# Performance work log

Measured on AMD Instinct MI355X. Metric: run time of the kernel, lower is better.

## Reference

```python
import jax, jax.numpy as jnp
import numpy as np

B, S, D = 4, 2048, 1024
H, DK, DV = 16, 64, 64


def setup_inputs() -> dict:
    key = jax.random.key(0)
    ks = jax.random.split(key, 7)
    scale = 0.02
    emb = jax.random.normal(ks[0], (B, S, D), dtype=jnp.float32)
    # per-head projection weights stacked over heads: [H, D, DK/DV]
    Wq = jax.random.normal(ks[1], (H, D, DK), dtype=jnp.float32) * scale
    Wk = jax.random.normal(ks[2], (H, D, DK), dtype=jnp.float32) * scale
    Wv = jax.random.normal(ks[3], (H, D, DV), dtype=jnp.float32) * scale
    # output projection (nn.Linear(d_model, d_model)): weight [D, D] (input-major) + bias
    Wo = jax.random.normal(ks[4], (D, D), dtype=jnp.float32) * scale
    bo = jax.random.normal(ks[5], (D,), dtype=jnp.float32) * scale
    return {"emb": emb, "Wq": Wq, "Wk": Wk, "Wv": Wv, "Wo": Wo, "bo": bo}


def reference(emb, Wq, Wk, Wv, Wo, bo):
    # Per-head projections, batched over heads: [B,H,S,dk]
    q = jnp.einsum("bsd,hdk->bhsk", emb, Wq)
    k = jnp.einsum("bsd,hdk->bhsk", emb, Wk)
    v = jnp.einsum("bsd,hdv->bhsv", emb, Wv)
    # Scaled dot-product with causal mask (bool_mask=True)
    scores = jnp.einsum("bhqk,bhsk->bhqs", q, k) * (DK ** -0.5)  # [B,H,S,S]
    causal = jnp.tril(jnp.ones((S, S), dtype=bool))
    scores = jnp.where(causal, scores, jnp.finfo(scores.dtype).min)
    attn = jax.nn.softmax(scores, axis=-1)
    out = jnp.einsum("bhqs,bhsv->bhqv", attn, v)  # [B,H,S,DV]
    # concat heads -> [B,S,H*DV] == [B,S,D]
    out = out.transpose(0, 2, 1, 3).reshape(B, S, H * DV)
    # output projection; dropout=0.0 -> identity
    return out @ Wo + bo
```

## Files before the change

kernel.cpp:

```cpp
#include <hip/hip_runtime.h>
#include <hip/hip_bf16.h>


typedef __attribute__((ext_vector_type(8))) short bf16x8;
typedef __attribute__((ext_vector_type(4))) float f32x4;
typedef __attribute__((ext_vector_type(4))) unsigned int u32x4;
typedef __attribute__((ext_vector_type(2))) unsigned int u32x2;

#define MFMA16(a, b, c) __builtin_amdgcn_mfma_f32_16x16x32_bf16((a), (b), (c), 0, 0, 0)

#define LOG2E 1.44269504088896340736f
#define BIG_NEG (-3.0e38f)
#define DEFER_THR 10.0f

__device__ __forceinline__ unsigned short f2bf(float f) {
  union { float f; unsigned int i; } x; x.f = f;
  unsigned int lsb = (x.i >> 16) & 1;
  x.i += 0x7fffu + lsb;
  return (unsigned short)(x.i >> 16);
}

__device__ __forceinline__ unsigned int cvtpk(float lo, float hi) {
  unsigned int r;
  asm("v_cvt_pk_bf16_f32 %0, %1, %2" : "=v"(r) : "v"(lo), "v"(hi));
  return r;
}

__device__ __forceinline__ void gl16(const unsigned short* g, void* l) {
  __builtin_amdgcn_global_load_lds(
      (const __attribute__((address_space(1))) unsigned int*)g,
      (__attribute__((address_space(3))) unsigned int*)l, 16, 0, 0);
}

__global__ void wtrans_kernel(const float* __restrict__ in,
                              unsigned short* __restrict__ out, int R, int C) {
  __shared__ unsigned short tile[32][33];
  const int bz = blockIdx.z;
  const int c0 = blockIdx.x * 32, r0 = blockIdx.y * 32;
  const float* ip = in + (size_t)bz * R * C;
  unsigned short* op = out + (size_t)bz * R * C;
  const int tx = threadIdx.x, ty = threadIdx.y;
#pragma unroll
  for (int i = 0; i < 32; i += 8)
    tile[ty + i][tx] = f2bf(ip[(size_t)(r0 + ty + i) * C + (c0 + tx)]);
  __syncthreads();
#pragma unroll
  for (int i = 0; i < 32; i += 8)
    op[(size_t)(c0 + ty + i) * R + (r0 + tx)] = tile[tx][ty + i];
}

__global__ __launch_bounds__(256)
void embconv_kernel(const float* __restrict__ in, unsigned short* __restrict__ out) {
  const int i = blockIdx.x * 256 + threadIdx.x;
  const float4 a = ((const float4*)in)[2 * i];
  const float4 b = ((const float4*)in)[2 * i + 1];
  union { unsigned short u[8]; u32x4 v; } p;
  p.u[0] = f2bf(a.x); p.u[1] = f2bf(a.y); p.u[2] = f2bf(a.z); p.u[3] = f2bf(a.w);
  p.u[4] = f2bf(b.x); p.u[5] = f2bf(b.y); p.u[6] = f2bf(b.z); p.u[7] = f2bf(b.w);
  ((u32x4*)out)[i] = p.v;
}

__global__ __launch_bounds__(256)
void qkv_kernel(const unsigned short* __restrict__ embB,
                const unsigned short* __restrict__ WqT,
                const unsigned short* __restrict__ WkT,
                const unsigned short* __restrict__ WvT,
                unsigned short* __restrict__ QG,
                unsigned short* __restrict__ KG,
                unsigned short* __restrict__ VtG) {
  const int nwg = gridDim.x;
  const int wg = blockIdx.x;
  const int swz = (wg & 7) * (nwg >> 3) + (wg >> 3);
  const int mb = swz / 24;
  const int rem = swz - mb * 24;
  const int t = rem >> 3;
  const int m0 = mb * 128;
  const int n0 = (rem & 7) * 128;
  const int b = m0 >> 11;
  const int sloc = m0 & 2047;
  const unsigned short* Wt =
      (t == 0 ? WqT : (t == 1 ? WkT : WvT)) + (size_t)(n0 >> 6) * 64 * 1024;

  __shared__ __align__(16) unsigned short As[128 * 32];
  __shared__ __align__(16) unsigned short Bs[128 * 32];

  const int tid = threadIdx.x;
  const int lane = tid & 63, w = tid >> 6;
  const int q4 = lane >> 4, l16 = lane & 15;
  const int lr = lane >> 2, lc = (lane & 3) * 8;

  f32x4 acc[4][4] = {};

  const unsigned short* ga0 = &embB[(size_t)(m0 + w * 32 + lr) * 1024 + lc];
  const unsigned short* ga1 = ga0 + 16 * 1024;
  const unsigned short* gb0 = &Wt[(size_t)(w * 32 + lr) * 1024 + lc];
  const unsigned short* gb1 = gb0 + 16 * 1024;
  char* la0 = (char*)As + w * 2048;
  char* lb0 = (char*)Bs + w * 2048;

  for (int k0 = 0; k0 < 1024; k0 += 32) {
    __syncthreads();
    gl16(ga0 + k0, la0);
    gl16(ga1 + k0, la0 + 1024);
    gl16(gb0 + k0, lb0);
    gl16(gb1 + k0, lb0 + 1024);
    __syncthreads();

    const unsigned short* PA = (t == 2) ? Bs : As;
    const unsigned short* PB = (t == 2) ? As : Bs;

    bf16x8 af[4], bfr[4];
#pragma unroll
    for (int ms = 0; ms < 4; ++ms)
      af[ms] = *(const bf16x8*)&PA[((w >> 1) * 64 + ms * 16 + l16) * 32 + q4 * 8];
#pragma unroll
    for (int js = 0; js < 4; ++js)
      bfr[js] = *(const bf16x8*)&PB[((w & 1) * 64 + js * 16 + l16) * 32 + q4 * 8];
    __builtin_amdgcn_s_setprio(1);
#pragma unroll
    for (int ms = 0; ms < 4; ++ms)
#pragma unroll
      for (int js = 0; js < 4; ++js)
        acc[ms][js] = MFMA16(af[ms], bfr[js], acc[ms][js]);
    __builtin_amdgcn_s_setprio(0);
  }

  if (t < 2) {
    unsigned short* outp = (t == 0) ? QG : KG;
    const float osc = (t == 0) ? (0.125f * LOG2E) : 1.0f;
    const int h = (n0 >> 6) + (w & 1);
    const size_t hb = (size_t)(b * 16 + h) * 2048;
#pragma unroll
    for (int ms = 0; ms < 4; ++ms)
#pragma unroll
      for (int js = 0; js < 4; ++js) {
        const int c = js * 16 + l16;
#pragma unroll
        for (int r = 0; r < 4; ++r) {
          const int s = sloc + (w >> 1) * 64 + ms * 16 + q4 * 4 + r;
          outp[(hb + s) * 64 + c] = f2bf(acc[ms][js][r] * osc);
        }
      }
  } else {
    const int h = (n0 >> 6) + (w >> 1);
    const size_t hb = (size_t)(b * 16 + h) * 64;
#pragma unroll
    for (int ms = 0; ms < 4; ++ms)
#pragma unroll
      for (int js = 0; js < 4; ++js) {
        const int s = sloc + (w & 1) * 64 + js * 16 + l16;
#pragma unroll
        for (int r = 0; r < 4; ++r) {
          const int c = ms * 16 + q4 * 4 + r;
          VtG[(hb + c) * 2048 + s] = f2bf(acc[ms][js][r]);
        }
      }
  }
}

__global__ __launch_bounds__(512)
void flash_kernel(const unsigned short* __restrict__ QG,
                  const unsigned short* __restrict__ KG,
                  const unsigned short* __restrict__ VtG,
                  unsigned short* __restrict__ ObG) {
  const int bh = blockIdx.x;
  const int y = blockIdx.y;
  const int k4 = y >> 2, y0 = y & 3;
  const int t = k4 + 4 * ((y0 + k4) & 3);
  const int q0 = t * 128;
  const int tid = threadIdx.x;
  const int lane = tid & 63, w = tid >> 6;
  const int wp = w & 3;
  const int q4 = lane >> 4, l16 = lane & 15;
  const int qw = q0 + w * 16;
  const int jlim = q0 + ((w >= 4) ? 64 : 0);
  const int jlimB = q0 + 64;

  const unsigned short* Qp = QG + ((size_t)bh * 2048 + qw) * 64;
  const unsigned short* Kp = KG + (size_t)bh * 2048 * 64;
  const unsigned short* Vp = VtG + (size_t)bh * 64 * 2048;

  const bf16x8 qf0 = *(const bf16x8*)&Qp[(size_t)l16 * 64 + q4 * 8];
  const bf16x8 qf1 = *(const bf16x8*)&Qp[(size_t)l16 * 64 + 32 + q4 * 8];

  __shared__ __align__(16) unsigned short Ks[64][72];
  __shared__ __align__(16) unsigned short Vs[64][72];
  __shared__ __align__(16) unsigned short Plds[8][16][72];

  f32x4 oacc[4] = {};
  float m_i = BIG_NEG, l_part = 0.f;

  const int sr = tid >> 3, sc = (tid & 7) * 8;
  u32x4 kreg = *(const u32x4*)&Kp[(size_t)sr * 64 + sc];
  u32x4 vreg = *(const u32x4*)&Vp[(size_t)sr * 2048 + sc];

  for (int j0 = 0; j0 <= jlimB; j0 += 64) {
    *(u32x4*)&Ks[sr][sc] = kreg;
    *(u32x4*)&Vs[sr][sc] = vreg;
    __syncthreads();

    if (j0 + 64 <= jlimB) {
      const int jn = j0 + 64;
      kreg = *(const u32x4*)&Kp[(size_t)(jn + sr) * 64 + sc];
      vreg = *(const u32x4*)&Vp[(size_t)sr * 2048 + jn + sc];
    }

    if (j0 <= jlim) {
      f32x4 sacc[4] = {};
      __builtin_amdgcn_s_setprio(1);
#pragma unroll
      for (int js = 0; js < 4; ++js) {
        const bf16x8 kf0 = *(const bf16x8*)&Ks[js * 16 + l16][q4 * 8];
        const bf16x8 kf1 = *(const bf16x8*)&Ks[js * 16 + l16][32 + q4 * 8];
        sacc[js] = MFMA16(kf0, qf0, sacc[js]);
        sacc[js] = MFMA16(kf1, qf1, sacc[js]);
      }
      __builtin_amdgcn_s_setprio(0);

      float mloc = BIG_NEG;
      if (j0 == jlim) {
        const int qrel = wp * 16 + l16;
#pragma unroll
        for (int js = 0; js < 4; ++js)
#pragma unroll
          for (int r = 0; r < 4; ++r) {
            const int krel = js * 16 + q4 * 4 + r;
            float v = sacc[js][r];
            if (krel > qrel) v = BIG_NEG;
            sacc[js][r] = v;
            mloc = fmaxf(mloc, v);
          }
      } else {
#pragma unroll
        for (int js = 0; js < 4; ++js)
#pragma unroll
          for (int r = 0; r < 4; ++r) mloc = fmaxf(mloc, sacc[js][r]);
      }
      mloc = fmaxf(mloc, __shfl_xor(mloc, 16, 64));
      mloc = fmaxf(mloc, __shfl_xor(mloc, 32, 64));

      if (__any(mloc > m_i + DEFER_THR)) {
        const float mnew = fmaxf(m_i, mloc);
        const float alpha = __builtin_amdgcn_exp2f(m_i - mnew);
        m_i = mnew;
        l_part *= alpha;
#pragma unroll
        for (int js = 0; js < 4; ++js)
#pragma unroll
          for (int r = 0; r < 4; ++r) oacc[js][r] *= alpha;
      }

#pragma unroll
      for (int js = 0; js < 4; ++js)
#pragma unroll
        for (int r = 0; r < 4; ++r) {
          const float p = __builtin_amdgcn_exp2f(sacc[js][r] - m_i);
          sacc[js][r] = p;
          l_part += p;
        }

#pragma unroll
      for (int js = 0; js < 4; ++js) {
        u32x2 pk;
        pk[0] = cvtpk(sacc[js][0], sacc[js][1]);
        pk[1] = cvtpk(sacc[js][2], sacc[js][3]);
        *(u32x2*)&Plds[w][l16][js * 16 + q4 * 4] = pk;
      }

      asm volatile("" ::: "memory");

      const bf16x8 pf0 = *(const bf16x8*)&Plds[w][l16][q4 * 8];
      const bf16x8 pf1 = *(const bf16x8*)&Plds[w][l16][32 + q4 * 8];

      __builtin_amdgcn_s_setprio(1);
#pragma unroll
      for (int js = 0; js < 4; ++js) {
        const bf16x8 vf0 = *(const bf16x8*)&Vs[js * 16 + l16][q4 * 8];
        const bf16x8 vf1 = *(const bf16x8*)&Vs[js * 16 + l16][32 + q4 * 8];
        oacc[js] = MFMA16(vf0, pf0, oacc[js]);
        oacc[js] = MFMA16(vf1, pf1, oacc[js]);
      }
      __builtin_amdgcn_s_setprio(0);
    }
    __syncthreads();
  }

  float l_i = l_part;
  l_i += __shfl_xor(l_i, 16, 64);
  l_i += __shfl_xor(l_i, 32, 64);

  const int b = bh >> 4, h = bh & 15;
  const int q = qw + l16;
  const float rl = 1.0f / l_i;
  unsigned short* orow = ObG + ((size_t)b * 2048 + q) * 1024 + h * 64;
#pragma unroll
  for (int js = 0; js < 4; ++js) {
    u32x2 ok;
    ok[0] = cvtpk(oacc[js][0] * rl, oacc[js][1] * rl);
    ok[1] = cvtpk(oacc[js][2] * rl, oacc[js][3] * rl);
    *(u32x2*)&orow[js * 16 + q4 * 4] = ok;
  }
}

__global__ __launch_bounds__(256)
void oproj_kernel(const unsigned short* __restrict__ ObG,
                  const unsigned short* __restrict__ WoT,
                  const float* __restrict__ bo,
                  float* __restrict__ outG) {
  const int nwg = gridDim.x;
  const int wg = blockIdx.x;
  const int swz = (wg & 7) * (nwg >> 3) + (wg >> 3);
  const int m0 = (swz >> 3) * 128;
  const int n0 = (swz & 7) * 128;

  __shared__ __align__(16) unsigned short As[128 * 32];
  __shared__ __align__(16) unsigned short Bs[128 * 32];

  const int tid = threadIdx.x;
  const int lane = tid & 63, w = tid >> 6;
  const int q4 = lane >> 4, l16 = lane & 15;
  const int lr = lane >> 2, lc = (lane & 3) * 8;

  f32x4 acc[4][4] = {};

  const unsigned short* ga0 = &ObG[(size_t)(m0 + w * 32 + lr) * 1024 + lc];
  const unsigned short* ga1 = ga0 + 16 * 1024;
  const unsigned short* gb0 = &WoT[(size_t)(n0 + w * 32 + lr) * 1024 + lc];
  const unsigned short* gb1 = gb0 + 16 * 1024;
  char* la0 = (char*)As + w * 2048;
  char* lb0 = (char*)Bs + w * 2048;

  for (int k0 = 0; k0 < 1024; k0 += 32) {
    __syncthreads();
    gl16(ga0 + k0, la0);
    gl16(ga1 + k0, la0 + 1024);
    gl16(gb0 + k0, lb0);
    gl16(gb1 + k0, lb0 + 1024);
    __syncthreads();

    bf16x8 af[4], bfr[4];
#pragma unroll
    for (int ms = 0; ms < 4; ++ms)
      af[ms] = *(const bf16x8*)&As[((w >> 1) * 64 + ms * 16 + l16) * 32 + q4 * 8];
#pragma unroll
    for (int js = 0; js < 4; ++js)
      bfr[js] = *(const bf16x8*)&Bs[((w & 1) * 64 + js * 16 + l16) * 32 + q4 * 8];
    __builtin_amdgcn_s_setprio(1);
#pragma unroll
    for (int ms = 0; ms < 4; ++ms)
#pragma unroll
      for (int js = 0; js < 4; ++js)
        acc[ms][js] = MFMA16(af[ms], bfr[js], acc[ms][js]);
    __builtin_amdgcn_s_setprio(0);
  }

#pragma unroll
  for (int js = 0; js < 4; ++js) {
    const int col = n0 + (w & 1) * 64 + js * 16 + l16;
    const float bias = bo[col];
#pragma unroll
    for (int ms = 0; ms < 4; ++ms)
#pragma unroll
      for (int r = 0; r < 4; ++r) {
        const int row = m0 + (w >> 1) * 64 + ms * 16 + q4 * 4 + r;
        outG[(size_t)row * 1024 + col] = acc[ms][js][r] + bias;
      }
  }
}

extern "C" void kernel_launch(void* const* d_in, const int* in_sizes, int n_in,
                              void* d_out, int out_size, void* d_ws, size_t ws_size,
                              hipStream_t stream) {
  const float* emb = (const float*)d_in[0];
  const float* Wq  = (const float*)d_in[1];
  const float* Wk  = (const float*)d_in[2];
  const float* Wv  = (const float*)d_in[3];
  const float* Wo  = (const float*)d_in[4];
  const float* bo  = (const float*)d_in[5];
  float* out = (float*)d_out;

  char* ws = (char*)d_ws;
  const size_t MB = 1024 * 1024;

  const int nb = (ws_size >= 72 * MB) ? 4 : (ws_size >= 40 * MB) ? 2 : 1;

  unsigned short* WqT = (unsigned short*)(ws + 0 * MB);
  unsigned short* WkT = (unsigned short*)(ws + 2 * MB);
  unsigned short* WvT = (unsigned short*)(ws + 4 * MB);
  unsigned short* WoT = (unsigned short*)(ws + 6 * MB);
  unsigned short* QG  = (unsigned short*)(ws + 8 * MB);
  unsigned short* KG  = (unsigned short*)(ws + (8 + 4 * nb) * MB);
  unsigned short* VtG = (unsigned short*)(ws + (8 + 8 * nb) * MB);
  unsigned short* ObG = (unsigned short*)(ws + (8 + 12 * nb) * MB);

  const dim3 tb(32, 8, 1);
  wtrans_kernel<<<dim3(2, 32, 16), tb, 0, stream>>>(Wq, WqT, 1024, 64);
  wtrans_kernel<<<dim3(2, 32, 16), tb, 0, stream>>>(Wk, WkT, 1024, 64);
  wtrans_kernel<<<dim3(2, 32, 16), tb, 0, stream>>>(Wv, WvT, 1024, 64);
  wtrans_kernel<<<dim3(32, 32, 1), tb, 0, stream>>>(Wo, WoT, 1024, 1024);

  for (int g = 0; g < 4; g += nb) {
    const float* embG = emb + (size_t)g * 2048 * 1024;
    float* outG = out + (size_t)g * 2048 * 1024;
    unsigned short* embB = ObG;
    embconv_kernel<<<dim3(nb * 1024), 256, 0, stream>>>(embG, embB);
    qkv_kernel<<<dim3(24 * 16 * nb), 256, 0, stream>>>(embB, WqT, WkT, WvT, QG, KG, VtG);
    flash_kernel<<<dim3(16 * nb, 16), 512, 0, stream>>>(QG, KG, VtG, ObG);
    oproj_kernel<<<dim3(8 * 16 * nb), 256, 0, stream>>>(ObG, WoT, bo, outG);
  }
}
```

Before: 280.4 us.

## Fuse emb fp32->bf16 conversion into QKV GEMM and pair causal flash tiles

The separate embedding conversion kernel is removed: the QKV GEMM now loads fp32 embeddings directly, converts them to bf16 in registers and stores them into a padded LDS tile, saving one full pass through global memory and one launch. The flash kernel moves from 512-thread blocks over 128-query tiles to 256-thread blocks that each process two 64-query tiles (p and 31-p), which balances causal work across blocks. In exchange, the A-operand load in the GEMM becomes a synchronous register path instead of direct-to-LDS loads, and the flash kernel runs the tiles sequentially with extra K/V reloads between phases.

```diff
diff --git a/kernel.cpp b/kernel.cpp
--- a/kernel.cpp
+++ b/kernel.cpp
@@ -49,19 +49,8 @@
     op[(size_t)(c0 + ty + i) * R + (r0 + tx)] = tile[tx][ty + i];
 }
 
-__global__ __launch_bounds__(256)
-void embconv_kernel(const float* __restrict__ in, unsigned short* __restrict__ out) {
-  const int i = blockIdx.x * 256 + threadIdx.x;
-  const float4 a = ((const float4*)in)[2 * i];
-  const float4 b = ((const float4*)in)[2 * i + 1];
-  union { unsigned short u[8]; u32x4 v; } p;
-  p.u[0] = f2bf(a.x); p.u[1] = f2bf(a.y); p.u[2] = f2bf(a.z); p.u[3] = f2bf(a.w);
-  p.u[4] = f2bf(b.x); p.u[5] = f2bf(b.y); p.u[6] = f2bf(b.z); p.u[7] = f2bf(b.w);
-  ((u32x4*)out)[i] = p.v;
-}
-
-__global__ __launch_bounds__(256)
-void qkv_kernel(const unsigned short* __restrict__ embB,
+__global__ __launch_bounds__(256, 4)
+void qkv_kernel(const float* __restrict__ embF,
                 const unsigned short* __restrict__ WqT,
                 const unsigned short* __restrict__ WkT,
                 const unsigned short* __restrict__ WvT,
@@ -81,41 +70,57 @@
   const unsigned short* Wt =
       (t == 0 ? WqT : (t == 1 ? WkT : WvT)) + (size_t)(n0 >> 6) * 64 * 1024;
 
-  __shared__ __align__(16) unsigned short As[128 * 32];
+  __shared__ __align__(16) unsigned short As[128][40];
   __shared__ __align__(16) unsigned short Bs[128 * 32];
 
   const int tid = threadIdx.x;
   const int lane = tid & 63, w = tid >> 6;
   const int q4 = lane >> 4, l16 = lane & 15;
   const int lr = lane >> 2, lc = (lane & 3) * 8;
+  const int arow = tid >> 1, acol = (tid & 1) * 16;
 
   f32x4 acc[4][4] = {};
 
-  const unsigned short* ga0 = &embB[(size_t)(m0 + w * 32 + lr) * 1024 + lc];
-  const unsigned short* ga1 = ga0 + 16 * 1024;
+  const float* aptr = &embF[(size_t)(m0 + arow) * 1024 + acol];
   const unsigned short* gb0 = &Wt[(size_t)(w * 32 + lr) * 1024 + lc];
   const unsigned short* gb1 = gb0 + 16 * 1024;
-  char* la0 = (char*)As + w * 2048;
   char* lb0 = (char*)Bs + w * 2048;
 
   for (int k0 = 0; k0 < 1024; k0 += 32) {
     __syncthreads();
-    gl16(ga0 + k0, la0);
-    gl16(ga1 + k0, la0 + 1024);
     gl16(gb0 + k0, lb0);
     gl16(gb1 + k0, lb0 + 1024);
+    {
+      const float4 v0 = *(const float4*)&aptr[k0];
+      const float4 v1 = *(const float4*)&aptr[k0 + 4];
+      const float4 v2 = *(const float4*)&aptr[k0 + 8];
+      const float4 v3 = *(const float4*)&aptr[k0 + 12];
+      u32x4 p0, p1;
+      p0[0] = cvtpk(v0.x, v0.y); p0[1] = cvtpk(v0.z, v0.w);
+      p0[2] = cvtpk(v1.x, v1.y); p0[3] = cvtpk(v1.z, v1.w);
+      p1[0] = cvtpk(v2.x, v2.y); p1[1] = cvtpk(v2.z, v2.w);
+      p1[2] = cvtpk(v3.x, v3.y); p1[3] = cvtpk(v3.z, v3.w);
+      *(u32x4*)&As[arow][acol]     = p0;
+      *(u32x4*)&As[arow][acol + 8] = p1;
+    }
     __syncthreads();
 
-    const unsigned short* PA = (t == 2) ? Bs : As;
-    const unsigned short* PB = (t == 2) ? As : Bs;
-
     bf16x8 af[4], bfr[4];
-#pragma unroll
-    for (int ms = 0; ms < 4; ++ms)
-      af[ms] = *(const bf16x8*)&PA[((w >> 1) * 64 + ms * 16 + l16) * 32 + q4 * 8];
-#pragma unroll
-    for (int js = 0; js < 4; ++js)
-      bfr[js] = *(const bf16x8*)&PB[((w & 1) * 64 + js * 16 + l16) * 32 + q4 * 8];
+    if (t == 2) {
+#pragma unroll
+      for (int ms = 0; ms < 4; ++ms)
+        af[ms] = *(const bf16x8*)&Bs[((w >> 1) * 64 + ms * 16 + l16) * 32 + q4 * 8];
+#pragma unroll
+      for (int js = 0; js < 4; ++js)
+        bfr[js] = *(const bf16x8*)&As[(w & 1) * 64 + js * 16 + l16][q4 * 8];
+    } else {
+#pragma unroll
+      for (int ms = 0; ms < 4; ++ms)
+        af[ms] = *(const bf16x8*)&As[(w >> 1) * 64 + ms * 16 + l16][q4 * 8];
+#pragma unroll
+      for (int js = 0; js < 4; ++js)
+        bfr[js] = *(const bf16x8*)&Bs[((w & 1) * 64 + js * 16 + l16) * 32 + q4 * 8];
+    }
     __builtin_amdgcn_s_setprio(1);
 #pragma unroll
     for (int ms = 0; ms < 4; ++ms)
@@ -158,54 +163,66 @@
   }
 }
 
-__global__ __launch_bounds__(512)
+__global__ __launch_bounds__(256, 4)
 void flash_kernel(const unsigned short* __restrict__ QG,
                   const unsigned short* __restrict__ KG,
                   const unsigned short* __restrict__ VtG,
                   unsigned short* __restrict__ ObG) {
   const int bh = blockIdx.x;
-  const int y = blockIdx.y;
-  const int k4 = y >> 2, y0 = y & 3;
-  const int t = k4 + 4 * ((y0 + k4) & 3);
-  const int q0 = t * 128;
+  const int p = blockIdx.y;
   const int tid = threadIdx.x;
   const int lane = tid & 63, w = tid >> 6;
-  const int wp = w & 3;
   const int q4 = lane >> 4, l16 = lane & 15;
-  const int qw = q0 + w * 16;
-  const int jlim = q0 + ((w >= 4) ? 64 : 0);
-  const int jlimB = q0 + 64;
-
-  const unsigned short* Qp = QG + ((size_t)bh * 2048 + qw) * 64;
+
   const unsigned short* Kp = KG + (size_t)bh * 2048 * 64;
   const unsigned short* Vp = VtG + (size_t)bh * 64 * 2048;
 
-  const bf16x8 qf0 = *(const bf16x8*)&Qp[(size_t)l16 * 64 + q4 * 8];
-  const bf16x8 qf1 = *(const bf16x8*)&Qp[(size_t)l16 * 64 + 32 + q4 * 8];
-
   __shared__ __align__(16) unsigned short Ks[64][72];
   __shared__ __align__(16) unsigned short Vs[64][72];
-  __shared__ __align__(16) unsigned short Plds[8][16][72];
-
-  f32x4 oacc[4] = {};
-  float m_i = BIG_NEG, l_part = 0.f;
-
-  const int sr = tid >> 3, sc = (tid & 7) * 8;
-  u32x4 kreg = *(const u32x4*)&Kp[(size_t)sr * 64 + sc];
-  u32x4 vreg = *(const u32x4*)&Vp[(size_t)sr * 2048 + sc];
-
-  for (int j0 = 0; j0 <= jlimB; j0 += 64) {
-    *(u32x4*)&Ks[sr][sc] = kreg;
-    *(u32x4*)&Vs[sr][sc] = vreg;
-    __syncthreads();
-
-    if (j0 + 64 <= jlimB) {
-      const int jn = j0 + 64;
-      kreg = *(const u32x4*)&Kp[(size_t)(jn + sr) * 64 + sc];
-      vreg = *(const u32x4*)&Vp[(size_t)sr * 2048 + jn + sc];
-    }
-
-    if (j0 <= jlim) {
+  __shared__ __align__(16) unsigned short Plds[4][16][72];
+
+  const int sr = tid >> 2, sc = (tid & 3) * 16;
+  u32x4 kr0, kr1, vr0, vr1;
+  {
+    kr0 = *(const u32x4*)&Kp[(size_t)sr * 64 + sc];
+    kr1 = *(const u32x4*)&Kp[(size_t)sr * 64 + sc + 8];
+    vr0 = *(const u32x4*)&Vp[(size_t)sr * 2048 + sc];
+    vr1 = *(const u32x4*)&Vp[(size_t)sr * 2048 + sc + 8];
+  }
+
+  const int xs0 = 31 - p, xs1 = p;
+#pragma unroll 1
+  for (int ph = 0; ph < 2; ++ph) {
+    const int q0 = (ph == 0 ? xs0 : xs1) * 64;
+    const int qw = q0 + w * 16;
+    const unsigned short* Qp = QG + ((size_t)bh * 2048 + qw) * 64;
+    const bf16x8 qf0 = *(const bf16x8*)&Qp[(size_t)l16 * 64 + q4 * 8];
+    const bf16x8 qf1 = *(const bf16x8*)&Qp[(size_t)l16 * 64 + 32 + q4 * 8];
+
+    f32x4 oacc[4] = {};
+    float m_i = BIG_NEG, l_part = 0.f;
+
+#pragma unroll 1
+    for (int j0 = 0; j0 <= q0; j0 += 64) {
+      *(u32x4*)&Ks[sr][sc]     = kr0;
+      *(u32x4*)&Ks[sr][sc + 8] = kr1;
+      *(u32x4*)&Vs[sr][sc]     = vr0;
+      *(u32x4*)&Vs[sr][sc + 8] = vr1;
+      __syncthreads();
+
+      if (j0 < q0) {
+        const int jn = j0 + 64;
+        kr0 = *(const u32x4*)&Kp[(size_t)(jn + sr) * 64 + sc];
+        kr1 = *(const u32x4*)&Kp[(size_t)(jn + sr) * 64 + sc + 8];
+        vr0 = *(const u32x4*)&Vp[(size_t)sr * 2048 + jn + sc];
+        vr1 = *(const u32x4*)&Vp[(size_t)sr * 2048 + jn + sc + 8];
+      } else if (ph == 0) {
+        kr0 = *(const u32x4*)&Kp[(size_t)sr * 64 + sc];
+        kr1 = *(const u32x4*)&Kp[(size_t)sr * 64 + sc + 8];
+        vr0 = *(const u32x4*)&Vp[(size_t)sr * 2048 + sc];
+        vr1 = *(const u32x4*)&Vp[(size_t)sr * 2048 + sc + 8];
+      }
+
       f32x4 sacc[4] = {};
       __builtin_amdgcn_s_setprio(1);
 #pragma unroll
@@ -218,8 +235,8 @@
       __builtin_amdgcn_s_setprio(0);
 
       float mloc = BIG_NEG;
-      if (j0 == jlim) {
-        const int qrel = wp * 16 + l16;
+      if (j0 == q0) {
+        const int qrel = w * 16 + l16;
 #pragma unroll
         for (int js = 0; js < 4; ++js)
 #pragma unroll
@@ -254,9 +271,9 @@
       for (int js = 0; js < 4; ++js)
 #pragma unroll
         for (int r = 0; r < 4; ++r) {
-          const float p = __builtin_amdgcn_exp2f(sacc[js][r] - m_i);
-          sacc[js][r] = p;
-          l_part += p;
+          const float pv = __builtin_amdgcn_exp2f(sacc[js][r] - m_i);
+          sacc[js][r] = pv;
+          l_part += pv;
         }
 
 #pragma unroll
@@ -281,24 +298,24 @@
         oacc[js] = MFMA16(vf1, pf1, oacc[js]);
       }
       __builtin_amdgcn_s_setprio(0);
+      __syncthreads();
     }
-    __syncthreads();
-  }
-
-  float l_i = l_part;
-  l_i += __shfl_xor(l_i, 16, 64);
-  l_i += __shfl_xor(l_i, 32, 64);
-
-  const int b = bh >> 4, h = bh & 15;
-  const int q = qw + l16;
-  const float rl = 1.0f / l_i;
-  unsigned short* orow = ObG + ((size_t)b * 2048 + q) * 1024 + h * 64;
-#pragma unroll
-  for (int js = 0; js < 4; ++js) {
-    u32x2 ok;
-    ok[0] = cvtpk(oacc[js][0] * rl, oacc[js][1] * rl);
-    ok[1] = cvtpk(oacc[js][2] * rl, oacc[js][3] * rl);
-    *(u32x2*)&orow[js * 16 + q4 * 4] = ok;
+
+    float l_i = l_part;
+    l_i += __shfl_xor(l_i, 16, 64);
+    l_i += __shfl_xor(l_i, 32, 64);
+
+    const int b = bh >> 4, h = bh & 15;
+    const int q = qw + l16;
+    const float rl = 1.0f / l_i;
+    unsigned short* orow = ObG + ((size_t)b * 2048 + q) * 1024 + h * 64;
+#pragma unroll
+    for (int js = 0; js < 4; ++js) {
+      u32x2 ok;
+      ok[0] = cvtpk(oacc[js][0] * rl, oacc[js][1] * rl);
+      ok[1] = cvtpk(oacc[js][2] * rl, oacc[js][3] * rl);
+      *(u32x2*)&orow[js * 16 + q4 * 4] = ok;
+    }
   }
 }
 
@@ -402,10 +419,8 @@
   for (int g = 0; g < 4; g += nb) {
     const float* embG = emb + (size_t)g * 2048 * 1024;
     float* outG = out + (size_t)g * 2048 * 1024;
-    unsigned short* embB = ObG;
-    embconv_kernel<<<dim3(nb * 1024), 256, 0, stream>>>(embG, embB);
-    qkv_kernel<<<dim3(24 * 16 * nb), 256, 0, stream>>>(embB, WqT, WkT, WvT, QG, KG, VtG);
-    flash_kernel<<<dim3(16 * nb, 16), 512, 0, stream>>>(QG, KG, VtG, ObG);
+    qkv_kernel<<<dim3(24 * 16 * nb), 256, 0, stream>>>(embG, WqT, WkT, WvT, QG, KG, VtG);
+    flash_kernel<<<dim3(16 * nb, 16), 256, 0, stream>>>(QG, KG, VtG, ObG);
     oproj_kernel<<<dim3(8 * 16 * nb), 256, 0, stream>>>(ObG, WoT, bo, outG);
   }
 }
```

After: 290.6 us. 3.6% more time.

## Fuse fp32-to-bf16 embedding conversion into QKV projection GEMM A-tile loads

Applied to the files above, without the earlier changes.

Removes the separate embconv kernel and has the QKV GEMM read fp32 embeddings directly, converting them to bf16 in registers before storing into a padded LDS tile. The next k-slice is prefetched into registers during the MFMA work. This saves a kernel launch and the bf16 write and read round trip of the embeddings. In exchange, each of the 24 N-tiles per M block now re-reads the fp32 rows, doubling A-side global traffic per tile, and the conversion runs repeatedly inside the GEMM.

```diff
diff --git a/kernel.cpp b/kernel.cpp
--- a/kernel.cpp
+++ b/kernel.cpp
@@ -50,18 +50,7 @@
 }
 
 __global__ __launch_bounds__(256)
-void embconv_kernel(const float* __restrict__ in, unsigned short* __restrict__ out) {
-  const int i = blockIdx.x * 256 + threadIdx.x;
-  const float4 a = ((const float4*)in)[2 * i];
-  const float4 b = ((const float4*)in)[2 * i + 1];
-  union { unsigned short u[8]; u32x4 v; } p;
-  p.u[0] = f2bf(a.x); p.u[1] = f2bf(a.y); p.u[2] = f2bf(a.z); p.u[3] = f2bf(a.w);
-  p.u[4] = f2bf(b.x); p.u[5] = f2bf(b.y); p.u[6] = f2bf(b.z); p.u[7] = f2bf(b.w);
-  ((u32x4*)out)[i] = p.v;
-}
-
-__global__ __launch_bounds__(256)
-void qkv_kernel(const unsigned short* __restrict__ embB,
+void qkv_kernel(const float* __restrict__ embF,
                 const unsigned short* __restrict__ WqT,
                 const unsigned short* __restrict__ WkT,
                 const unsigned short* __restrict__ WvT,
@@ -81,41 +70,65 @@
   const unsigned short* Wt =
       (t == 0 ? WqT : (t == 1 ? WkT : WvT)) + (size_t)(n0 >> 6) * 64 * 1024;
 
-  __shared__ __align__(16) unsigned short As[128 * 32];
+  __shared__ __align__(16) unsigned short As[128][40];
   __shared__ __align__(16) unsigned short Bs[128 * 32];
 
   const int tid = threadIdx.x;
   const int lane = tid & 63, w = tid >> 6;
   const int q4 = lane >> 4, l16 = lane & 15;
   const int lr = lane >> 2, lc = (lane & 3) * 8;
+  const int arow = tid >> 1, acol = (tid & 1) * 16;
 
   f32x4 acc[4][4] = {};
 
-  const unsigned short* ga0 = &embB[(size_t)(m0 + w * 32 + lr) * 1024 + lc];
-  const unsigned short* ga1 = ga0 + 16 * 1024;
+  const float* aptr = &embF[(size_t)(m0 + arow) * 1024 + acol];
   const unsigned short* gb0 = &Wt[(size_t)(w * 32 + lr) * 1024 + lc];
   const unsigned short* gb1 = gb0 + 16 * 1024;
-  char* la0 = (char*)As + w * 2048;
   char* lb0 = (char*)Bs + w * 2048;
 
+  float4 v0 = *(const float4*)&aptr[0];
+  float4 v1 = *(const float4*)&aptr[4];
+  float4 v2 = *(const float4*)&aptr[8];
+  float4 v3 = *(const float4*)&aptr[12];
+
   for (int k0 = 0; k0 < 1024; k0 += 32) {
     __syncthreads();
-    gl16(ga0 + k0, la0);
-    gl16(ga1 + k0, la0 + 1024);
+    {
+      u32x4 p0, p1;
+      p0[0] = cvtpk(v0.x, v0.y); p0[1] = cvtpk(v0.z, v0.w);
+      p0[2] = cvtpk(v1.x, v1.y); p0[3] = cvtpk(v1.z, v1.w);
+      p1[0] = cvtpk(v2.x, v2.y); p1[1] = cvtpk(v2.z, v2.w);
+      p1[2] = cvtpk(v3.x, v3.y); p1[3] = cvtpk(v3.z, v3.w);
+      *(u32x4*)&As[arow][acol]     = p0;
+      *(u32x4*)&As[arow][acol + 8] = p1;
+    }
     gl16(gb0 + k0, lb0);
     gl16(gb1 + k0, lb0 + 1024);
     __syncthreads();
 
-    const unsigned short* PA = (t == 2) ? Bs : As;
-    const unsigned short* PB = (t == 2) ? As : Bs;
+    if (k0 + 32 < 1024) {
+      v0 = *(const float4*)&aptr[k0 + 32];
+      v1 = *(const float4*)&aptr[k0 + 36];
+      v2 = *(const float4*)&aptr[k0 + 40];
+      v3 = *(const float4*)&aptr[k0 + 44];
+    }
 
     bf16x8 af[4], bfr[4];
-#pragma unroll
-    for (int ms = 0; ms < 4; ++ms)
-      af[ms] = *(const bf16x8*)&PA[((w >> 1) * 64 + ms * 16 + l16) * 32 + q4 * 8];
-#pragma unroll
-    for (int js = 0; js < 4; ++js)
-      bfr[js] = *(const bf16x8*)&PB[((w & 1) * 64 + js * 16 + l16) * 32 + q4 * 8];
+    if (t == 2) {
+#pragma unroll
+      for (int ms = 0; ms < 4; ++ms)
+        af[ms] = *(const bf16x8*)&Bs[((w >> 1) * 64 + ms * 16 + l16) * 32 + q4 * 8];
+#pragma unroll
+      for (int js = 0; js < 4; ++js)
+        bfr[js] = *(const bf16x8*)&As[(w & 1) * 64 + js * 16 + l16][q4 * 8];
+    } else {
+#pragma unroll
+      for (int ms = 0; ms < 4; ++ms)
+        af[ms] = *(const bf16x8*)&As[(w >> 1) * 64 + ms * 16 + l16][q4 * 8];
+#pragma unroll
+      for (int js = 0; js < 4; ++js)
+        bfr[js] = *(const bf16x8*)&Bs[((w & 1) * 64 + js * 16 + l16) * 32 + q4 * 8];
+    }
     __builtin_amdgcn_s_setprio(1);
 #pragma unroll
     for (int ms = 0; ms < 4; ++ms)
@@ -402,9 +415,7 @@
   for (int g = 0; g < 4; g += nb) {
     const float* embG = emb + (size_t)g * 2048 * 1024;
     float* outG = out + (size_t)g * 2048 * 1024;
-    unsigned short* embB = ObG;
-    embconv_kernel<<<dim3(nb * 1024), 256, 0, stream>>>(embG, embB);
-    qkv_kernel<<<dim3(24 * 16 * nb), 256, 0, stream>>>(embB, WqT, WkT, WvT, QG, KG, VtG);
+    qkv_kernel<<<dim3(24 * 16 * nb), 256, 0, stream>>>(embG, WqT, WkT, WvT, QG, KG, VtG);
     flash_kernel<<<dim3(16 * nb, 16), 512, 0, stream>>>(QG, KG, VtG, ObG);
     oproj_kernel<<<dim3(8 * 16 * nb), 256, 0, stream>>>(ObG, WoT, bo, outG);
   }
```

Result: slower. 318.5 us (+13.6%).
